# Optimization experiments

Measured on AMD Instinct MI355X. Metric: run time of the kernel, lower is better.

## Reference

```python
import jax, jax.numpy as jnp
import numpy as np


def _conv(x, w, b=None, stride=1, pad=0):
    # x: [N,C,H,W], w: [O,I,kh,kw]
    out = jax.lax.conv_general_dilated(
        x, w, (stride, stride), [(pad, pad), (pad, pad)],
        dimension_numbers=('NCHW', 'OIHW', 'NCHW'))
    return out if b is None else out + b[None, :, None, None]


def _cond_net(x, cw1, cb1, cw2, cb2, cw3, cb3):
    # ZeroPad2d(1) + conv(pad=0) == conv(pad=1)
    h = jax.nn.relu(_conv(x, cw1, cb1, stride=2, pad=1))
    h = jax.nn.relu(_conv(h, cw2, cb2, stride=2, pad=1))
    h = jax.nn.relu(_conv(h, cw3, cb3, stride=2, pad=1))
    return h.mean(axis=(2, 3))  # [B, 32]


def _hda(x, dyn_w, ow, share_w, share_b):
    # per-sample dynamic conv: weight[b] = dyn_w * ow[b]
    B = x.shape[0]
    w = dyn_w[None] * ow.reshape(B, *dyn_w.shape)  # [B,32,64,3,3]
    out1 = jax.vmap(lambda xb, wb: _conv(xb[None], wb, pad=1)[0])(x, w)
    out2 = _conv(x, share_w, share_b, pad=1)
    return jnp.concatenate([out1, out2], axis=1)  # [B,64,H,W]


def setup_inputs() -> dict:
    key = jax.random.key(0)
    ks = jax.random.split(key, 20)
    s = 0.05
    inp = {
        'x': jax.random.normal(ks[0], (8, 64, 256, 256), jnp.float32),
        'out_weight1': jax.random.normal(ks[1], (256, 64, 3, 3), jnp.float32),
        'out_weight2': jax.random.normal(ks[2], (256, 64, 3, 3), jnp.float32),
        # Condition_tp params
        'cw1': jax.random.normal(ks[3], (32, 64, 7, 7), jnp.float32) * s,
        'cb1': jnp.zeros((32,), jnp.float32),
        'cw2': jax.random.normal(ks[4], (32, 32, 3, 3), jnp.float32) * s,
        'cb2': jnp.zeros((32,), jnp.float32),
        'cw3': jax.random.normal(ks[5], (32, 32, 3, 3), jnp.float32) * s,
        'cb3': jnp.zeros((32,), jnp.float32),
        # FiLM linears (cond_nf=32 -> base_nf=64)
        'scale_w': jax.random.normal(ks[6], (64, 32), jnp.float32) * s,
        'scale_b': jnp.zeros((64,), jnp.float32),
        'shift_w': jax.random.normal(ks[7], (64, 32), jnp.float32) * s,
        'shift_b': jnp.zeros((64,), jnp.float32),
        # HDA_conv 1
        'dyn1_w': jax.random.normal(ks[8], (32, 64, 3, 3), jnp.float32) * s,
        'share1_w': jax.random.normal(ks[9], (32, 64, 3, 3), jnp.float32) * s,
        'share1_b': jnp.zeros((32,), jnp.float32),
        # HDA_conv 2
        'dyn2_w': jax.random.normal(ks[10], (32, 64, 3, 3), jnp.float32) * s,
        'share2_w': jax.random.normal(ks[11], (32, 64, 3, 3), jnp.float32) * s,
        'share2_b': jnp.zeros((32,), jnp.float32),
    }
    return inp


def reference(x, out_weight1, out_weight2, cw1, cb1, cw2, cb2, cw3, cb3,
              scale_w, scale_b, shift_w, shift_b,
              dyn1_w, share1_w, share1_b, dyn2_w, share2_w, share2_b):
    res_scale = 1.0
    cond = _cond_net(x, cw1, cb1, cw2, cb2, cw3, cb3)       # [B,32]
    scale = cond @ scale_w.T + scale_b                      # [B,64]
    shift = cond @ shift_w.T + shift_b                      # [B,64]
    out = _hda(x, dyn1_w, out_weight1, share1_w, share1_b)  # [B,64,H,W]
    # out*scale + shift + out  ==  out*(scale+1) + shift
    out = out * (scale[:, :, None, None] + 1.0) + shift[:, :, None, None]
    out = jax.nn.relu(out)
    out = _hda(out, dyn2_w, out_weight2, share2_w, share2_b)
    return x + out * res_scale
```

## Files before the change

### kernel.cpp

```cpp
#include <hip/hip_runtime.h>

typedef unsigned short u16;
typedef unsigned int u32;
typedef __attribute__((ext_vector_type(8))) __bf16 bf16x8;
typedef __attribute__((ext_vector_type(8))) u16 u16x8;
typedef __attribute__((ext_vector_type(4))) float f32x4;
typedef __attribute__((ext_vector_type(2))) u32 u32x2;

static constexpr size_t PSP = (size_t)8 * 258 * 258 * 16;

#define GPTR(p) ((const __attribute__((address_space(1))) void*)(p))
#define LPTR(p) ((__attribute__((address_space(3))) void*)(p))

__device__ __forceinline__ u16 f2bf(float f) {
  u32 u = __builtin_bit_cast(u32, f);
  u = (u + 0x7FFFu + ((u >> 16) & 1u)) >> 16;
  return (u16)u;
}

__device__ __forceinline__ f32x4 mfma16(bf16x8 a, bf16x8 b, f32x4 c) {
  return __builtin_amdgcn_mfma_f32_16x16x32_bf16(a, b, c, 0, 0, 0);
}

__global__ void k_zero_border(u16* __restrict__ base) {
  int idx = blockIdx.x * 256 + threadIdx.x;
  if (idx >= 4 * 8 * 1028) return;
  int p = idx / (8 * 1028), r = idx - p * (8 * 1028);
  int b = r / 1028, e = r - b * 1028;
  int y, x;
  if (e < 258) { y = 0; x = e; }
  else if (e < 516) { y = 257; x = e - 258; }
  else { int e2 = e - 516; y = 1 + (e2 >> 1); x = (e2 & 1) * 257; }
  u16* d = base + (size_t)p * PSP + (((size_t)b * 258 + y) * 258 + x) * 16;
  u16x8 z = (u16x8)0;
  *(u16x8*)d = z;
  *(u16x8*)(d + 8) = z;
}

__global__ __launch_bounds__(256) void k_tr(const float* __restrict__ x,
                                            u16* __restrict__ xh) {
  __shared__ float t[64][33];
  const int b = blockIdx.z, y = blockIdx.y, x0 = blockIdx.x * 32;
  const int tid = threadIdx.x;
  {
    int ic = tid >> 2, xo = (tid & 3) * 8;
    const float* s = x + (((size_t)b * 64 + ic) * 256 + y) * 256 + x0 + xo;
    f32x4 v0 = *(const f32x4*)s;
    f32x4 v1 = *(const f32x4*)(s + 4);
#pragma unroll
    for (int j = 0; j < 4; ++j) { t[ic][xo + j] = v0[j]; t[ic][xo + 4 + j] = v1[j]; }
  }
  __syncthreads();
  {
    int xc = tid & 31, slot = tid >> 5;
    int ic0 = slot * 8;
    u16x8 v;
#pragma unroll
    for (int j = 0; j < 8; ++j) v[j] = f2bf(t[ic0 + j][xc]);
    *(u16x8*)(xh + (size_t)(slot >> 1) * PSP +
              (((size_t)b * 258 + y + 1) * 258 + x0 + xc + 1) * 16 + (slot & 1) * 8) = v;
  }
}

__global__ void k_prep_cw(const float* __restrict__ src, u16* __restrict__ dst,
                          int IC, int KK2, int n, int perm) {
  int d = blockIdx.x * 256 + threadIdx.x;
  if (d >= n) return;
  int per = KK2 * IC;
  int oc = d / per, r = d - oc * per;
  int tap = r / IC, icp = r - tap * IC;
  int ic = perm ? ((icp >> 1) + (icp & 1) * 16) : icp;
  dst[d] = f2bf(src[(oc * IC + ic) * KK2 + tap]);
}

__global__ void k_prep_cw1(const float* __restrict__ src, u16* __restrict__ dst) {
  int d = blockIdx.x * 256 + threadIdx.x;
  if (d >= 106496) return;
  int h = d / 13312, r = d - h * 13312;
  int t = r >> 8, r2 = r & 255;
  int oc = r2 >> 3, i = r2 & 7;
  float v = (t < 49) ? src[(oc * 64 + h * 8 + i) * 49 + t] : 0.f;
  dst[d] = f2bf(v);
}

__global__ void k_prep_hda(const float* __restrict__ dyn, const float* __restrict__ ow,
                           const float* __restrict__ share, const float* __restrict__ a_,
                           u16* __restrict__ dst, int use_a, int perm) {
  int d = blockIdx.x * 256 + threadIdx.x;
  if (d >= 327680) return;
  int b = d / 40960, r = d - b * 40960;
  int cc = r / 10240, r2 = r - cc * 10240;
  int oc = r2 / 160, r3 = r2 - oc * 160;
  int s = r3 >> 5, r4 = r3 & 31;
  int kq = r4 >> 3, j = r4 & 7;
  int tap = 2 * s + (kq >> 1);
  float v = 0.f;
  if (tap < 9) {
    int icp = cc * 16 + (kq & 1) * 8 + j;
    int ic = perm ? ((icp & 3) * 16 + (icp >> 2)) : icp;
    v = (oc < 32) ? dyn[(oc * 64 + ic) * 9 + tap] * ow[((b * 32 + oc) * 64 + ic) * 9 + tap]
                  : share[((oc - 32) * 64 + ic) * 9 + tap];
    if (use_a) v *= a_[b * 64 + oc];
  }
  dst[d] = f2bf(v);
}

__global__ __launch_bounds__(256, 2) void k_cond1_mfma(const u16* __restrict__ xh,
    const u16* __restrict__ wp , const float* __restrict__ cb,
    u16* __restrict__ dst) {
  __shared__ char lds[49152];
  const int wg0 = blockIdx.x;
  const int wg = ((wg0 & 7) << 6) | (wg0 >> 3);
  const int b = wg >> 6, rr = wg & 63;
  const int oh0 = (rr >> 3) << 4, ow0 = (rr & 7) << 4;
  const int tid = threadIdx.x, lane = tid & 63, wid = tid >> 6;
  const int col = lane & 15, kq = lane >> 4;
  f32x4 acc[4][2];
#pragma unroll
  for (int i = 0; i < 4; ++i)
#pragma unroll
    for (int j = 0; j < 2; ++j) acc[i][j] = 0.f;
  int pb[4];
#pragma unroll
  for (int mf = 0; mf < 4; ++mf) pb[mf] = (2 * (wid * 4 + mf)) * 37 + 2 * col;
#pragma unroll 1
  for (int h = 0; h < 8; ++h) {
    __syncthreads();
#pragma unroll
    for (int it = 0; it < 6; ++it) {
      if (it < 5 || wid < 2) {
        int g = it * 256 + tid;
        int i = g ^ ((g >> 3) & 7);
        if (i >= 1406) i = 0;
        int r = i / 37, cc2 = i - r * 37;
        const u16* src = xh + (size_t)(h >> 1) * PSP +
            (((size_t)b * 258 + 2 * oh0 + r) * 258 + 2 * ow0 + cc2) * 16 + (h & 1) * 8;
        __builtin_amdgcn_global_load_lds(GPTR(src),
            LPTR(lds + (it * 256 + wid * 64) * 16), 16, 0, 0);
      }
    }
#pragma unroll
    for (int it = 0; it < 7; ++it) {
      if (it < 6 || wid < 2) {
        int g = it * 256 + tid;
        int t = g >> 5, oc = g & 31;
        const u16* src = wp + h * 13312 + t * 256 + oc * 8;
        __builtin_amdgcn_global_load_lds(GPTR(src),
            LPTR(lds + 22528 + (it * 256 + wid * 64) * 16), 16, 0, 0);
      }
    }
    __syncthreads();
    __builtin_amdgcn_s_setprio(1);
#pragma unroll
    for (int s = 0; s < 13; ++s) {
      const int t0 = 4 * s;
      const int kh0 = t0 / 7, r7 = t0 % 7;
      int carry = (kq >= 7 - r7) ? 1 : 0;
      int kh = kh0 + carry;
      int kw = r7 + kq - carry * 7;
      int prow = kh * 37 + kw;
      bf16x8 a[4];
#pragma unroll
      for (int mf = 0; mf < 4; ++mf) {
        int pos = pb[mf] + prow;
        int g = pos ^ ((pos >> 3) & 7);
        a[mf] = __builtin_bit_cast(bf16x8, *(const u16x8*)(lds + g * 16));
      }
      bf16x8 w[2];
#pragma unroll
      for (int nf = 0; nf < 2; ++nf)
        w[nf] = __builtin_bit_cast(bf16x8,
            *(const u16x8*)(lds + 22528 + (((4 * s + kq) * 32) + nf * 16 + col) * 16));
#pragma unroll
      for (int mf = 0; mf < 4; ++mf)
#pragma unroll
        for (int nf = 0; nf < 2; ++nf) acc[mf][nf] = mfma16(a[mf], w[nf], acc[mf][nf]);
    }
    __builtin_amdgcn_s_setprio(0);
  }
  const float bv0 = cb[col], bv1 = cb[16 + col];
#pragma unroll
  for (int mf = 0; mf < 4; ++mf) {
    int oh = oh0 + wid * 4 + mf;
    if (oh >= 126) continue;
#pragma unroll
    for (int r = 0; r < 4; ++r) {
      int ow = ow0 + kq * 4 + r;
      if (ow >= 126) continue;
      u32 pack = (u32)f2bf(fmaxf(acc[mf][0][r] + bv0, 0.f)) |
                 ((u32)f2bf(fmaxf(acc[mf][1][r] + bv1, 0.f)) << 16);
      *(u32*)(dst + (((size_t)b * 126 + oh) * 126 + ow) * 32 + col * 2) = pack;
    }
  }
}

template <int HI, int HO, int IC, int KK, int OUTF32>
__global__ __launch_bounds__(256, 4) void k_conv_s2(const u16* __restrict__ src,
    const u16* __restrict__ wgt, const float* __restrict__ bias, void* __restrict__ dst) {
  const int b = blockIdx.z;
  const int by0 = blockIdx.y * 8, bx0 = blockIdx.x * 16;
  const int tid = threadIdx.x, lane = tid & 63, wid = tid >> 6;
  const int col = lane & 15, kq = lane >> 4;
  f32x4 acc[2][2];
#pragma unroll
  for (int i = 0; i < 2; ++i)
#pragma unroll
    for (int j = 0; j < 2; ++j) acc[i][j] = 0.f;
  const u16x8 Z = (u16x8)0;
#pragma unroll
  for (int kh = 0; kh < KK; ++kh) {
#pragma unroll
    for (int kw = 0; kw < KK; ++kw) {
#pragma unroll
      for (int h = 0; h < IC / 32; ++h) {
        bf16x8 a[2];
#pragma unroll
        for (int mf = 0; mf < 2; ++mf) {
          int oh = by0 + wid * 2 + mf;
          int ih = 2 * oh - 1 + kh;
          int ix = 2 * (bx0 + col) - 1 + kw;
          int ic = h * 32 + kq * 8;
          u16x8 raw = Z;
          if ((unsigned)ih < (unsigned)HI && (unsigned)ix < (unsigned)HI)
            raw = *(const u16x8*)(src + (((size_t)b * HI + ih) * HI + ix) * IC + ic);
          a[mf] = __builtin_bit_cast(bf16x8, raw);
        }
        int k0 = (kh * KK + kw) * IC + h * 32 + kq * 8;
        bf16x8 w[2];
#pragma unroll
        for (int nf = 0; nf < 2; ++nf)
          w[nf] = __builtin_bit_cast(bf16x8,
                    *(const u16x8*)(wgt + (size_t)(nf * 16 + col) * (KK * KK * IC) + k0));
#pragma unroll
        for (int mf = 0; mf < 2; ++mf)
#pragma unroll
          for (int nf = 0; nf < 2; ++nf) acc[mf][nf] = mfma16(a[mf], w[nf], acc[mf][nf]);
      }
    }
  }
#pragma unroll
  for (int mf = 0; mf < 2; ++mf) {
    int oh = by0 + wid * 2 + mf;
    if (oh >= HO) continue;
#pragma unroll
    for (int nf = 0; nf < 2; ++nf) {
      int oc = nf * 16 + col;
      float bv = bias[oc];
#pragma unroll
      for (int r = 0; r < 4; ++r) {
        int ow = bx0 + kq * 4 + r;
        if (ow >= HO) continue;
        float v = fmaxf(acc[mf][nf][r] + bv, 0.f);
        if (OUTF32)
          ((float*)dst)[(((size_t)b * 32 + oc) * HO + oh) * HO + ow] = v;
        else
          ((u16*)dst)[(((size_t)b * HO + oh) * HO + ow) * 32 + oc] = f2bf(v);
      }
    }
  }
}

__global__ void k_mean(const float* __restrict__ h3, float* __restrict__ cond) {
  int bo = blockIdx.x;
  int tid = threadIdx.x;
  float s = 0.f;
  for (int i = tid; i < 1024; i += 256) s += h3[bo * 1024 + i];
  __shared__ float red[256];
  red[tid] = s;
  __syncthreads();
  for (int o = 128; o > 0; o >>= 1) {
    if (tid < o) red[tid] += red[tid + o];
    __syncthreads();
  }
  if (tid == 0) cond[bo] = red[0] * (1.f / 1024.f);
}

__global__ void k_film(const float* __restrict__ cond,
                       const float* __restrict__ scale_w, const float* __restrict__ scale_b,
                       const float* __restrict__ shift_w, const float* __restrict__ shift_b,
                       const float* __restrict__ share1_b, const float* __restrict__ share2_b,
                       float* __restrict__ a_, float* __restrict__ bias1,
                       float* __restrict__ bias2) {
  int t = threadIdx.x;
  int b = t >> 6, j = t & 63;
  float s = scale_b[j], sh = shift_b[j];
  for (int k = 0; k < 32; ++k) {
    float c = cond[b * 32 + k];
    s = fmaf(c, scale_w[j * 32 + k], s);
    sh = fmaf(c, shift_w[j * 32 + k], sh);
  }
  float a = s + 1.f;
  float b0 = (j < 32) ? 0.f : share1_b[j - 32];
  a_[t] = a;
  bias1[t] = fmaf(a, b0, sh);
  bias2[t] = (j < 32) ? 0.f : share2_b[j - 32];
}

__device__ __forceinline__ void hda_stage(const u16* __restrict__ asrc,
                                          const u16* __restrict__ wall,
                                          char* lb, int b, int by0, int bx0,
                                          int cc, int tid, int wid) {
  const u16* ap = asrc + (size_t)cc * PSP;
  const u16* wp = wall + (size_t)b * 40960 + cc * 10240;
#pragma unroll
  for (int it = 0; it < 2; ++it) {
    if (it == 0 || tid < 192) {
      int g = it * 512 + tid;
      int i = g ^ ((g >> 3) & 1);
      int pos = i >> 1, sl = i & 1;
      if (pos >= 342) { pos = 0; sl = 0; }
      int yy = pos / 18, xx = pos - yy * 18;
      const u16* src = ap + (((size_t)b * 258 + by0 + yy) * 258 + bx0 + xx) * 16 + sl * 8;
      __builtin_amdgcn_global_load_lds(GPTR(src),
          LPTR(lb + (it * 512 + wid * 64) * 16), 16, 0, 0);
    }
  }
#pragma unroll
  for (int it = 0; it < 3; ++it) {
    if (it < 2 || tid < 320) {
      int g = it * 512 + tid;
      int oc = g / 21, t = g - oc * 21;
      if (t > 19) t = 19;
      const u16* src = wp + oc * 160 + t * 8;
      __builtin_amdgcn_global_load_lds(GPTR(src),
          LPTR(lb + 11264 + (it * 512 + wid * 64) * 16), 16, 0, 0);
    }
  }
}

template <int STAGE>
__global__ __launch_bounds__(512, 2) void k_hda_mfma(const u16* __restrict__ asrc,
    const u16* __restrict__ wall, const float* __restrict__ bias,
    const float* __restrict__ resid, void* __restrict__ dst) {
  __shared__ char lds[65536];
  const int wg0 = blockIdx.x;
  const int wg = ((wg0 & 7) << 8) + (wg0 >> 3);
  const int b = wg >> 8;
  const int rr = wg & 255;
  const int by0 = (rr >> 4) << 4, bx0 = (rr & 15) << 4;
  const int tid = threadIdx.x, lane = tid & 63, wid = tid >> 6;
  const int col = lane & 15, kq = lane >> 4;
  const int hi = kq >> 1, sl2 = kq & 1;
  f32x4 acc[2][4];
#pragma unroll
  for (int i = 0; i < 2; ++i)
#pragma unroll
    for (int j = 0; j < 4; ++j) acc[i][j] = 0.f;
  hda_stage(asrc, wall, lds, b, by0, bx0, 0, tid, wid);
#pragma unroll
  for (int cc = 0; cc < 4; ++cc) {
    __syncthreads();
    if (cc < 3)
      hda_stage(asrc, wall, lds + ((cc + 1) & 1) * 32768, b, by0, bx0, cc + 1, tid, wid);
    char* lb = lds + (cc & 1) * 32768;
    __builtin_amdgcn_s_setprio(1);
#pragma unroll
    for (int s = 0; s < 5; ++s) {
      const int t0 = 2 * s, t1 = 2 * s + 1;
      const int d0 = (t0 / 3) * 18 + (t0 % 3);
      const int d1 = (t1 / 3) * 18 + (t1 % 3);
      const int dd = hi ? d1 : d0;
      bf16x8 a[2];
#pragma unroll
      for (int mf = 0; mf < 2; ++mf) {
        int pos = (wid * 2 + mf) * 18 + col + dd;
        int g = (pos * 2 + sl2) ^ ((pos >> 2) & 1);
        a[mf] = __builtin_bit_cast(bf16x8, *(const u16x8*)(lb + g * 16));
      }
      bf16x8 w[4];
#pragma unroll
      for (int nf = 0; nf < 4; ++nf)
        w[nf] = __builtin_bit_cast(bf16x8,
            *(const u16x8*)(lb + 11264 + (nf * 16 + col) * 336 + (s * 4 + kq) * 16));
#pragma unroll
      for (int mf = 0; mf < 2; ++mf)
#pragma unroll
        for (int nf = 0; nf < 4; ++nf) acc[mf][nf] = mfma16(a[mf], w[nf], acc[mf][nf]);
    }
    __builtin_amdgcn_s_setprio(0);
  }
  const float* bb = bias + b * 64;
#pragma unroll
  for (int mf = 0; mf < 2; ++mf) {
    int y = by0 + wid * 2 + mf;
    if (STAGE == 1) {
#pragma unroll
      for (int r = 0; r < 4; ++r) {
        int x = bx0 + kq * 4 + r;
        u32x2 pk;
        pk[0] = (u32)f2bf(fmaxf(acc[mf][0][r] + bb[col], 0.f)) |
                ((u32)f2bf(fmaxf(acc[mf][1][r] + bb[16 + col], 0.f)) << 16);
        pk[1] = (u32)f2bf(fmaxf(acc[mf][2][r] + bb[32 + col], 0.f)) |
                ((u32)f2bf(fmaxf(acc[mf][3][r] + bb[48 + col], 0.f)) << 16);
        *(u32x2*)((u16*)dst + (size_t)(col >> 2) * PSP +
                  (((size_t)b * 258 + y + 1) * 258 + x + 1) * 16 + (col & 3) * 4) = pk;
      }
    } else {
#pragma unroll
      for (int nf = 0; nf < 4; ++nf) {
        int oc = nf * 16 + col;
        float bv = bb[oc];
        size_t o = (((size_t)b * 64 + oc) * 256 + y) * 256 + bx0 + kq * 4;
        f32x4 rx = *(const f32x4*)(resid + o);
        f32x4 vv;
#pragma unroll
        for (int r = 0; r < 4; ++r) vv[r] = rx[r] + acc[mf][nf][r] + bv;
        *(f32x4*)((float*)dst + o) = vv;
      }
    }
  }
}

extern "C" void kernel_launch(void* const* d_in, const int* in_sizes, int n_in,
                              void* d_out, int out_size, void* d_ws, size_t ws_size,
                              hipStream_t stream) {
  const float* x        = (const float*)d_in[0];
  const float* ow1      = (const float*)d_in[1];
  const float* ow2      = (const float*)d_in[2];
  const float* cw1      = (const float*)d_in[3];
  const float* cb1      = (const float*)d_in[4];
  const float* cw2      = (const float*)d_in[5];
  const float* cb2      = (const float*)d_in[6];
  const float* cw3      = (const float*)d_in[7];
  const float* cb3      = (const float*)d_in[8];
  const float* scale_w  = (const float*)d_in[9];
  const float* scale_b  = (const float*)d_in[10];
  const float* shift_w  = (const float*)d_in[11];
  const float* shift_b  = (const float*)d_in[12];
  const float* dyn1     = (const float*)d_in[13];
  const float* share1   = (const float*)d_in[14];
  const float* share1_b = (const float*)d_in[15];
  const float* dyn2     = (const float*)d_in[16];
  const float* share2   = (const float*)d_in[17];
  const float* share2_b = (const float*)d_in[18];
  float* out = (float*)d_out;

  char* p = (char*)d_ws;
  u16* xh   = (u16*)p;            p += PSP * 4 * 2;
  u16* midh = (u16*)p;            p += PSP * 4 * 2;
  u16* wbf1 = (u16*)p;            p += (size_t)327680 * 2;
  u16* wbf2 = (u16*)p;            p += (size_t)327680 * 2;
  u16* cwb1 = (u16*)p;            p += (size_t)106496 * 2;
  u16* cwb2 = (u16*)p;            p += (size_t)32 * 288 * 2;
  u16* cwb3 = (u16*)p;            p += (size_t)32 * 288 * 2;
  float* a_    = (float*)p;       p += 512 * 4;
  float* bias1 = (float*)p;       p += 512 * 4;
  float* bias2 = (float*)p;       p += 512 * 4;
  float* cond  = (float*)p;       p += 256 * 4;
  u16* h1h = midh;
  u16* h2h = h1h + (size_t)8 * 126 * 126 * 32;
  float* h3 = (float*)(h2h + (size_t)8 * 63 * 63 * 32);

  k_zero_border<<<129, 256, 0, stream>>>(xh);
  k_tr<<<dim3(8, 256, 8), 256, 0, stream>>>(x, xh);

  k_prep_cw1<<<(106496 + 255) / 256, 256, 0, stream>>>(cw1, cwb1);
  k_prep_cw<<<(32 * 288 + 255) / 256, 256, 0, stream>>>(cw2, cwb2, 32, 9, 32 * 288, 1);
  k_prep_cw<<<(32 * 288 + 255) / 256, 256, 0, stream>>>(cw3, cwb3, 32, 9, 32 * 288, 0);

  k_cond1_mfma<<<512, 256, 0, stream>>>(xh, cwb1, cb1, h1h);
  k_conv_s2<126, 63, 32, 3, 0><<<dim3(4, 8, 8), 256, 0, stream>>>(h1h, cwb2, cb2, h2h);
  k_conv_s2<63, 32, 32, 3, 1><<<dim3(2, 4, 8), 256, 0, stream>>>(h2h, cwb3, cb3, h3);

  k_mean<<<256, 256, 0, stream>>>(h3, cond);
  k_film<<<1, 512, 0, stream>>>(cond, scale_w, scale_b, shift_w, shift_b,
                                share1_b, share2_b, a_, bias1, bias2);

  k_zero_border<<<129, 256, 0, stream>>>(midh);

  k_prep_hda<<<(327680 + 255) / 256, 256, 0, stream>>>(dyn1, ow1, share1, a_, wbf1, 1, 0);
  k_prep_hda<<<(327680 + 255) / 256, 256, 0, stream>>>(dyn2, ow2, share2, a_, wbf2, 0, 1);

  k_hda_mfma<1><<<2048, 512, 0, stream>>>(xh, wbf1, bias1, nullptr, midh);
  k_hda_mfma<2><<<2048, 512, 0, stream>>>(midh, wbf2, bias2, x, out);
}
```

Baseline: 248.6 us.

## Split HDA conv K-loop into 8-channel stages with triple-buffered LDS pipeline

The HDA MFMA kernel now runs K in eight stages of 8 input channels instead of four of 16. Weights are repacked so each MFMA k-group holds four taps of one 8-channel slice (12 padded taps), and a three-buffer LDS ring keeps two stages in flight using explicit vmcnt waits plus a raw barrier. A dummy load keeps the per-thread load count uniform for the waitcnt. This aims to hide global latency better and drop the XOR swizzle, but it pads more taps (12 vs 10 per 16 channels), adds more MFMA work per stage, and adds barriers.

```diff
diff --git a/kernel.cpp b/kernel.cpp
--- a/kernel.cpp
+++ b/kernel.cpp
@@ -87,16 +87,16 @@
                            const float* __restrict__ share, const float* __restrict__ a_,
                            u16* __restrict__ dst, int use_a, int perm) {
   int d = blockIdx.x * 256 + threadIdx.x;
-  if (d >= 327680) return;
-  int b = d / 40960, r = d - b * 40960;
-  int cc = r / 10240, r2 = r - cc * 10240;
-  int oc = r2 / 160, r3 = r2 - oc * 160;
+  if (d >= 393216) return;
+  int b = d / 49152, r = d - b * 49152;
+  int cc = r / 6144, r2 = r - cc * 6144;
+  int oc = r2 / 96, r3 = r2 - oc * 96;
   int s = r3 >> 5, r4 = r3 & 31;
   int kq = r4 >> 3, j = r4 & 7;
-  int tap = 2 * s + (kq >> 1);
+  int tap = 4 * s + kq;
   float v = 0.f;
   if (tap < 9) {
-    int icp = cc * 16 + (kq & 1) * 8 + j;
+    int icp = cc * 8 + j;
     int ic = perm ? ((icp & 3) * 16 + (icp >> 2)) : icp;
     v = (oc < 32) ? dyn[(oc * 64 + ic) * 9 + tap] * ow[((b * 32 + oc) * 64 + ic) * 9 + tap]
                   : share[((oc - 32) * 64 + ic) * 9 + tap];
@@ -296,34 +296,30 @@
   bias2[t] = (j < 32) ? 0.f : share2_b[j - 32];
 }
 
-__device__ __forceinline__ void hda_stage(const u16* __restrict__ asrc,
-                                          const u16* __restrict__ wall,
-                                          char* lb, int b, int by0, int bx0,
-                                          int cc, int tid, int wid) {
-  const u16* ap = asrc + (size_t)cc * PSP;
-  const u16* wp = wall + (size_t)b * 40960 + cc * 10240;
-#pragma unroll
-  for (int it = 0; it < 2; ++it) {
-    if (it == 0 || tid < 192) {
-      int g = it * 512 + tid;
-      int i = g ^ ((g >> 3) & 1);
-      int pos = i >> 1, sl = i & 1;
-      if (pos >= 342) { pos = 0; sl = 0; }
-      int yy = pos / 18, xx = pos - yy * 18;
-      const u16* src = ap + (((size_t)b * 258 + by0 + yy) * 258 + bx0 + xx) * 16 + sl * 8;
-      __builtin_amdgcn_global_load_lds(GPTR(src),
-          LPTR(lb + (it * 512 + wid * 64) * 16), 16, 0, 0);
-    }
-  }
+__device__ __forceinline__ void hda_stage8(const u16* __restrict__ asrc,
+                                           const u16* __restrict__ wall,
+                                           char* lds, int buf, int b, int by0, int bx0,
+                                           int cc, int wid, int lane) {
+  char* lb = lds + buf * 19456;
+  const u16* ap = asrc + (size_t)(cc >> 1) * PSP;
+  const u16* wp = wall + (size_t)b * 49152 + cc * 6144;
 #pragma unroll
   for (int it = 0; it < 3; ++it) {
-    if (it < 2 || tid < 320) {
-      int g = it * 512 + tid;
-      int oc = g / 21, t = g - oc * 21;
-      if (t > 19) t = 19;
-      const u16* src = wp + oc * 160 + t * 8;
-      __builtin_amdgcn_global_load_lds(GPTR(src),
-          LPTR(lb + 11264 + (it * 512 + wid * 64) * 16), 16, 0, 0);
+    int i = wid + 8 * it;
+    if (i < 6) {
+      int g = i * 64 + lane;
+      int pos = g < 342 ? g : 0;
+      int r = pos / 18, c = pos - r * 18;
+      const u16* src = ap + (((size_t)b * 258 + by0 + r) * 258 + bx0 + c) * 16 + (cc & 1) * 8;
+      __builtin_amdgcn_global_load_lds(GPTR(src), LPTR(lb + g * 16), 16, 0, 0);
+    } else if (i < 19) {
+      int g = (i - 6) * 64 + lane;
+      int oc = g / 13, t = g - oc * 13;
+      if (t > 11) t = 11;
+      const u16* src = wp + oc * 96 + t * 8;
+      __builtin_amdgcn_global_load_lds(GPTR(src), LPTR(lb + 6144 + g * 16), 16, 0, 0);
+    } else {
+      __builtin_amdgcn_global_load_lds(GPTR(wall), LPTR(lds + 58368 + lane * 16), 16, 0, 0);
     }
   }
 }
@@ -332,7 +328,7 @@
 __global__ __launch_bounds__(512, 2) void k_hda_mfma(const u16* __restrict__ asrc,
     const u16* __restrict__ wall, const float* __restrict__ bias,
     const float* __restrict__ resid, void* __restrict__ dst) {
-  __shared__ char lds[65536];
+  __shared__ char lds[59392];
   const int wg0 = blockIdx.x;
   const int wg = ((wg0 & 7) << 8) + (wg0 >> 3);
   const int b = wg >> 8;
@@ -340,38 +336,40 @@
   const int by0 = (rr >> 4) << 4, bx0 = (rr & 15) << 4;
   const int tid = threadIdx.x, lane = tid & 63, wid = tid >> 6;
   const int col = lane & 15, kq = lane >> 4;
-  const int hi = kq >> 1, sl2 = kq & 1;
   f32x4 acc[2][4];
 #pragma unroll
   for (int i = 0; i < 2; ++i)
 #pragma unroll
     for (int j = 0; j < 4; ++j) acc[i][j] = 0.f;
-  hda_stage(asrc, wall, lds, b, by0, bx0, 0, tid, wid);
-#pragma unroll
-  for (int cc = 0; cc < 4; ++cc) {
-    __syncthreads();
-    if (cc < 3)
-      hda_stage(asrc, wall, lds + ((cc + 1) & 1) * 32768, b, by0, bx0, cc + 1, tid, wid);
-    char* lb = lds + (cc & 1) * 32768;
+  hda_stage8(asrc, wall, lds, 0, b, by0, bx0, 0, wid, lane);
+  hda_stage8(asrc, wall, lds, 1, b, by0, bx0, 1, wid, lane);
+#pragma unroll
+  for (int cc = 0; cc < 8; ++cc) {
+    if (cc < 7)
+      asm volatile("s_waitcnt vmcnt(3)" ::: "memory");
+    else
+      asm volatile("s_waitcnt vmcnt(0)" ::: "memory");
+    __builtin_amdgcn_s_barrier();
+    if (cc < 6)
+      hda_stage8(asrc, wall, lds, (cc + 2) % 3, b, by0, bx0, cc + 2, wid, lane);
+    const char* lb = lds + (cc % 3) * 19456;
     __builtin_amdgcn_s_setprio(1);
 #pragma unroll
-    for (int s = 0; s < 5; ++s) {
-      const int t0 = 2 * s, t1 = 2 * s + 1;
-      const int d0 = (t0 / 3) * 18 + (t0 % 3);
-      const int d1 = (t1 / 3) * 18 + (t1 % 3);
-      const int dd = hi ? d1 : d0;
+    for (int s = 0; s < 3; ++s) {
+      int t = 4 * s + kq;
+      int kh = (t >= 3) + (t >= 6) + (t >= 9);
+      int dtap = kh * 18 + (t - kh * 3);
       bf16x8 a[2];
 #pragma unroll
       for (int mf = 0; mf < 2; ++mf) {
-        int pos = (wid * 2 + mf) * 18 + col + dd;
-        int g = (pos * 2 + sl2) ^ ((pos >> 2) & 1);
-        a[mf] = __builtin_bit_cast(bf16x8, *(const u16x8*)(lb + g * 16));
+        int pos = (wid * 2 + mf) * 18 + col + dtap;
+        a[mf] = __builtin_bit_cast(bf16x8, *(const u16x8*)(lb + pos * 16));
       }
       bf16x8 w[4];
 #pragma unroll
       for (int nf = 0; nf < 4; ++nf)
         w[nf] = __builtin_bit_cast(bf16x8,
-            *(const u16x8*)(lb + 11264 + (nf * 16 + col) * 336 + (s * 4 + kq) * 16));
+            *(const u16x8*)(lb + 6144 + (nf * 16 + col) * 208 + t * 16));
 #pragma unroll
       for (int mf = 0; mf < 2; ++mf)
 #pragma unroll
@@ -438,8 +436,8 @@
   char* p = (char*)d_ws;
   u16* xh   = (u16*)p;            p += PSP * 4 * 2;
   u16* midh = (u16*)p;            p += PSP * 4 * 2;
-  u16* wbf1 = (u16*)p;            p += (size_t)327680 * 2;
-  u16* wbf2 = (u16*)p;            p += (size_t)327680 * 2;
+  u16* wbf1 = (u16*)p;            p += (size_t)393216 * 2;
+  u16* wbf2 = (u16*)p;            p += (size_t)393216 * 2;
   u16* cwb1 = (u16*)p;            p += (size_t)106496 * 2;
   u16* cwb2 = (u16*)p;            p += (size_t)32 * 288 * 2;
   u16* cwb3 = (u16*)p;            p += (size_t)32 * 288 * 2;
@@ -468,8 +466,8 @@
 
   k_zero_border<<<129, 256, 0, stream>>>(midh);
 
-  k_prep_hda<<<(327680 + 255) / 256, 256, 0, stream>>>(dyn1, ow1, share1, a_, wbf1, 1, 0);
-  k_prep_hda<<<(327680 + 255) / 256, 256, 0, stream>>>(dyn2, ow2, share2, a_, wbf2, 0, 1);
+  k_prep_hda<<<(393216 + 255) / 256, 256, 0, stream>>>(dyn1, ow1, share1, a_, wbf1, 1, 0);
+  k_prep_hda<<<(393216 + 255) / 256, 256, 0, stream>>>(dyn2, ow2, share2, a_, wbf2, 0, 1);
 
   k_hda_mfma<1><<<2048, 512, 0, stream>>>(xh, wbf1, bias1, nullptr, midh);
   k_hda_mfma<2><<<2048, 512, 0, stream>>>(midh, wbf2, bias2, x, out);
```

Result: slower. 261.0 us (+5.0%).
